# Performance work log

Measured on AMD Instinct MI355X. Metric: run time of the kernel, lower is better.

## Reference

```python
import jax, jax.numpy as jnp
import numpy as np

TOP_K = 2
HORIZON = 10


def _lstm_layer(seq, w_ih, w_hh, b_ih, b_hh):
    """Single torch-style LSTM layer over seq [T, in]; returns hidden seq [T, hid]."""
    hid = w_hh.shape[1]
    def step(carry, x_t):
        h, c = carry
        z = x_t @ w_ih.T + h @ w_hh.T + b_ih + b_hh  # [4*hid], torch gate order i,f,g,o
        i, f, g, o = jnp.split(z, 4)
        c = jax.nn.sigmoid(f) * c + jax.nn.sigmoid(i) * jnp.tanh(g)
        h = jax.nn.sigmoid(o) * jnp.tanh(c)
        return (h, c), h
    init = (jnp.zeros((hid,), seq.dtype), jnp.zeros((hid,), seq.dtype))
    _, hs = jax.lax.scan(step, init, seq)
    return hs


def setup_inputs() -> dict:
    key = jax.random.key(0)
    ks = jax.random.split(key, 12)
    H, E = 4096, 64
    B, S = 4, 4096
    s = 0.02
    return {
        "x": jax.random.normal(ks[0], (B, S, H), jnp.float32),
        "gate_w": jax.random.normal(ks[1], (E, H), jnp.float32) * s,
        "expert_bias": jnp.zeros((E,), jnp.float32),
        "cp_w1": jax.random.normal(ks[2], (64, H), jnp.float32) * s,
        "cp_b1": jnp.zeros((64,), jnp.float32),
        "cp_w2": jax.random.normal(ks[3], (1, 64), jnp.float32) * s,
        "cp_b2": jnp.zeros((1,), jnp.float32),
        "load_buffer": jax.random.uniform(ks[4], (50, E), jnp.float32),
        "lp_w_ih0": jax.random.normal(ks[5], (256, E), jnp.float32) * s,
        "lp_w_hh0": jax.random.normal(ks[6], (256, 64), jnp.float32) * s,
        "lp_b_ih0": jnp.zeros((256,), jnp.float32),
        "lp_b_hh0": jnp.zeros((256,), jnp.float32),
        "lp_w_ih1": jax.random.normal(ks[7], (256, 64), jnp.float32) * s,
        "lp_w_hh1": jax.random.normal(ks[8], (256, 64), jnp.float32) * s,
        "lp_b_ih1": jnp.zeros((256,), jnp.float32),
        "lp_b_hh1": jnp.zeros((256,), jnp.float32),
        "head_w": jax.random.normal(ks[9], (E * HORIZON, 64), jnp.float32) * s,
        "head_b": jnp.zeros((E * HORIZON,), jnp.float32),
    }


def reference(x, gate_w, expert_bias, cp_w1, cp_b1, cp_w2, cp_b2, load_buffer,
              lp_w_ih0, lp_w_hh0, lp_b_ih0, lp_b_hh0,
              lp_w_ih1, lp_w_hh1, lp_b_ih1, lp_b_hh1, head_w, head_b):
    sg = jax.lax.stop_gradient
    B, S, H = x.shape
    E = gate_w.shape[0]
    flat = x.reshape(-1, H)                       # [N, H]
    N = flat.shape[0]

    # --- routing logits (small gate GEMM) ---
    logits = flat @ gate_w.T                      # [N, E]

    # --- LSTM load prediction (torch.no_grad in original) ---
    seq = sg(load_buffer)
    h1 = _lstm_layer(seq, sg(lp_w_ih0), sg(lp_w_hh0), sg(lp_b_ih0), sg(lp_b_hh0))
    h2 = _lstm_layer(h1, sg(lp_w_ih1), sg(lp_w_hh1), sg(lp_b_ih1), sg(lp_b_hh1))
    pred = h2[-1] @ sg(head_w).T + sg(head_b)     # [E*HORIZON]
    future_load = jax.nn.softmax(pred.reshape(E, HORIZON).mean(axis=1))  # [E]

    # --- bias + predicted-load adjustment, softmax, top-k ---
    adj_logits = logits + expert_bias - sg(future_load)
    probs = jax.nn.softmax(adj_logits, axis=-1)   # [N, E]
    top_scores, top_idx = jax.lax.top_k(probs, TOP_K)
    top_scores = top_scores / top_scores.sum(axis=-1, keepdims=True)

    # --- switch-style load-balancing auxiliary loss ---
    one_hot = jax.nn.one_hot(top_idx, E, dtype=probs.dtype)   # [N, k, E]
    f = one_hot.sum(axis=(0, 1)) / (N * TOP_K)                # routed fraction per expert
    P = probs.mean(axis=0)                                    # mean routing prob
    aux_loss = E * jnp.sum(f * P)

    # --- dynamic capacity from complexity predictor (torch.no_grad) ---
    comp = jax.nn.sigmoid(
        jax.nn.relu(flat @ sg(cp_w1).T + sg(cp_b1)) @ sg(cp_w2).T + sg(cp_b2))  # [N,1]
    capacity = jnp.clip(0.5 + 1.5 * comp.mean(), 0.5, 2.0)

    return top_scores, top_idx, aux_loss, capacity, future_load
```

## Files before the change

### kernel.cpp

```cpp
#include <hip/hip_runtime.h>
#include <stdint.h>

#define IMG_OFF_BYTES 80000
#define CHUNK_IMG 16384
#define LOGITS_OFF 680000
#define TAU 1e-3f

#define XLOFF 5120
#define BUF_STRIDE 10240

typedef __attribute__((ext_vector_type(8))) short short8v;
typedef __attribute__((ext_vector_type(4))) short short4v;
typedef __attribute__((ext_vector_type(4))) float f32x4;

__device__ __forceinline__ float rlf(float v, int l) {
  return __int_as_float(__builtin_amdgcn_readlane(__float_as_int(v), l));
}
__device__ __forceinline__ float wsum(float v) {
#pragma unroll
  for (int o = 32; o; o >>= 1) v += __shfl_xor(v, o, 64);
  return v;
}
__device__ __forceinline__ float wmax(float v) {
#pragma unroll
  for (int o = 32; o; o >>= 1) v = fmaxf(v, __shfl_xor(v, o, 64));
  return v;
}
__device__ __forceinline__ unsigned short f2bf(float f) {
  unsigned u = __float_as_uint(f);
  u += 0x7fffu + ((u >> 16) & 1u);
  return (unsigned short)(u >> 16);
}
__device__ __forceinline__ float bf2f(unsigned short h) {
  return __uint_as_float(((unsigned)h) << 16);
}
__device__ __forceinline__ short8v frag8(const char* p0, const char* p1) {
  short4v a = *(const short4v*)p0;
  short4v b = *(const short4v*)p1;
  return __builtin_shufflevector(a, b, 0, 1, 2, 3, 4, 5, 6, 7);
}

__device__ __forceinline__ void lds_barrier() {
  asm volatile("s_waitcnt lgkmcnt(0)" ::: "memory");
  __builtin_amdgcn_s_barrier();
  asm volatile("" ::: "memory");
  __builtin_amdgcn_sched_barrier(0);
}

__global__ __launch_bounds__(256) void prep_kernel(
    const float* __restrict__ gate_w, const float* __restrict__ cp_w1,
    float* __restrict__ ws)
{
  const int c = blockIdx.x;
  const int tid = threadIdx.x;
  if (c == 0 && tid < 144) ws[64 + tid] = 0.f;
  {
    float4 z = make_float4(0.f, 0.f, 0.f, 0.f);
    float4* lz = (float4*)(ws + LOGITS_OFF + c * 16384);
#pragma unroll
    for (int i = 0; i < 16; ++i) lz[tid + i * 256] = z;
  }
  const int row = tid >> 1;
  const int half = tid & 1;
  const float* src = ((row < 64) ? (gate_w + (size_t)row * 4096)
                                 : (cp_w1 + (size_t)(row - 64) * 4096)) + c * 32 + half * 16;
  float v[16];
#pragma unroll
  for (int j = 0; j < 4; ++j) *(float4*)&v[j * 4] = *(const float4*)(src + j * 4);
  const int g = row >> 4, r15 = row & 15;
  char* img = (char*)ws + IMG_OFF_BYTES + (size_t)c * CHUNK_IMG + g * 2048;
#pragma unroll
  for (int q = 0; q < 4; ++q) {
    unsigned short h0 = f2bf(v[4 * q + 0]), h1 = f2bf(v[4 * q + 1]);
    unsigned short h2 = f2bf(v[4 * q + 2]), h3 = f2bf(v[4 * q + 3]);
    unsigned short l0 = f2bf(v[4 * q + 0] - bf2f(h0));
    unsigned short l1 = f2bf(v[4 * q + 1] - bf2f(h1));
    unsigned short l2 = f2bf(v[4 * q + 2] - bf2f(h2));
    unsigned short l3 = f2bf(v[4 * q + 3] - bf2f(h3));
    uint2 hv, lv;
    hv.x = (unsigned)h0 | ((unsigned)h1 << 16);
    hv.y = (unsigned)h2 | ((unsigned)h3 << 16);
    lv.x = (unsigned)l0 | ((unsigned)l1 << 16);
    lv.y = (unsigned)l2 | ((unsigned)l3 << 16);
    const int l = q * 16 + r15;
    *(uint2*)(img + l * 16 + half * 8) = hv;
    *(uint2*)(img + 1024 + l * 16 + half * 8) = lv;
  }
}

__device__ void lstm_device(
    char* ldsbase,
    const float* __restrict__ lb,
    const float* __restrict__ wih0, const float* __restrict__ whh0,
    const float* __restrict__ bih0, const float* __restrict__ bhh0,
    const float* __restrict__ wih1, const float* __restrict__ whh1,
    const float* __restrict__ bih1, const float* __restrict__ bhh1,
    const float* __restrict__ head_w, const float* __restrict__ head_b,
    float* __restrict__ ws, float* __restrict__ out, int N)
{
  float* seqh = (float*)ldsbase;
  float* h1s  = seqh + 3200;
  float* zbuf = h1s + 3200;
  float* hbuf = zbuf + 256;
  float* preds = hbuf + 64;
  const int tid = threadIdx.x;
  const int lane = tid & 63;
  for (int i = tid; i < 3200; i += 256) seqh[i] = lb[i];

  float hv = 0.f;
#pragma unroll 1
  for (int L = 0; L < 2; ++L) {
    const float* wip  = L ? wih1 : wih0;
    const float* whp  = L ? whh1 : whh0;
    const float* bip  = L ? bih1 : bih0;
    const float* bhp  = L ? bhh1 : bhh0;
    const float* seqp = L ? h1s  : seqh;
    float wiR[64], whR[64];
#pragma unroll
    for (int j = 0; j < 64; j += 4) {
      *(float4*)&wiR[j] = *(const float4*)(wip + tid * 64 + j);
      *(float4*)&whR[j] = *(const float4*)(whp + tid * 64 + j);
    }
    const float bsum = bip[tid] + bhp[tid];
    float c_reg = 0.f;
    hv = 0.f;
    if (tid < 64) hbuf[tid] = 0.f;
    __syncthreads();
#pragma unroll 1
    for (int t = 0; t < 50; ++t) {
      const float xv = seqp[t * 64 + lane];
      float a0 = bsum, a1 = 0.f, a2 = 0.f, a3 = 0.f;
#pragma unroll
      for (int j = 0; j < 64; j += 4) {
        a0 = fmaf(rlf(xv, j + 0), wiR[j + 0], a0);
        a1 = fmaf(rlf(xv, j + 1), wiR[j + 1], a1);
        a2 = fmaf(rlf(xv, j + 2), wiR[j + 2], a2);
        a3 = fmaf(rlf(xv, j + 3), wiR[j + 3], a3);
      }
#pragma unroll
      for (int j = 0; j < 64; j += 4) {
        a0 = fmaf(rlf(hv, j + 0), whR[j + 0], a0);
        a1 = fmaf(rlf(hv, j + 1), whR[j + 1], a1);
        a2 = fmaf(rlf(hv, j + 2), whR[j + 2], a2);
        a3 = fmaf(rlf(hv, j + 3), whR[j + 3], a3);
      }
      zbuf[tid] = (a0 + a1) + (a2 + a3);
      __syncthreads();
      if (tid < 64) {
        const float zi = zbuf[tid], zf = zbuf[64 + tid];
        const float zg = zbuf[128 + tid], zo = zbuf[192 + tid];
        const float si = 1.f / (1.f + expf(-zi));
        const float sf = 1.f / (1.f + expf(-zf));
        const float so = 1.f / (1.f + expf(-zo));
        c_reg = sf * c_reg + si * tanhf(zg);
        const float h = so * tanhf(c_reg);
        hbuf[tid] = h;
        if (L == 0) h1s[t * 64 + tid] = h;
      }
      __syncthreads();
      hv = hbuf[lane];
    }
    __syncthreads();
  }
  for (int o = tid; o < 640; o += 256) {
    const float* hw = head_w + o * 64;
    float a0 = 0.f, a1 = 0.f, a2 = 0.f, a3 = 0.f;
#pragma unroll
    for (int j = 0; j < 64; j += 4) {
      a0 = fmaf(rlf(hv, j + 0), hw[j + 0], a0);
      a1 = fmaf(rlf(hv, j + 1), hw[j + 1], a1);
      a2 = fmaf(rlf(hv, j + 2), hw[j + 2], a2);
      a3 = fmaf(rlf(hv, j + 3), hw[j + 3], a3);
    }
    preds[o] = (a0 + a1) + (a2 + a3) + head_b[o];
  }
  __syncthreads();
  if (tid < 64) {
    float m = 0.f;
#pragma unroll
    for (int h = 0; h < 10; ++h) m += preds[tid * 10 + h];
    m = m / 10.f;
    const float mx = wmax(m);
    const float p = expf(m - mx);
    const float s = wsum(p);
    const float flv = p / s;
    ws[tid] = flv;
    out[4 * N + 2 + tid] = flv;
  }
}

__global__ __launch_bounds__(256) void gemm_kernel(
    const float* __restrict__ x, float* __restrict__ ws, float* __restrict__ out,
    const float* __restrict__ lb,
    const float* __restrict__ wih0, const float* __restrict__ whh0,
    const float* __restrict__ bih0, const float* __restrict__ bhh0,
    const float* __restrict__ wih1, const float* __restrict__ whh1,
    const float* __restrict__ bih1, const float* __restrict__ bhh1,
    const float* __restrict__ head_w, const float* __restrict__ head_b,
    int N)
{
  __shared__ __align__(16) char lds[30720];
  if (blockIdx.x == 0) {
    lstm_device(lds, lb, wih0, whh0, bih0, bhh0, wih1, whh1, bih1, bhh1,
                head_w, head_b, ws, out, N);
    return;
  }
  const int b = blockIdx.x - 1;
  const int tb = (b & 255) * 64;
  const int ck0 = (b >> 8) * 32;
  const int tid = threadIdx.x;
  const int lane = tid & 63;
  const int wv = __builtin_amdgcn_readfirstlane(tid >> 6);
  const int r15 = lane & 15;
  const int fo = (lane >> 4) * 8;
  const int row = tid >> 2;
  const int kslot = tid & 3;
  const float* xsrc = x + (size_t)(tb + row) * 4096 + kslot * 8;
  const char* wimg = (const char*)ws + IMG_OFF_BYTES;
  char* buf0 = lds;
  char* buf1 = lds + BUF_STRIDE;

  f32x4 acc[4][2];
#pragma unroll
  for (int mi = 0; mi < 4; ++mi)
#pragma unroll
    for (int ni = 0; ni < 2; ++ni) acc[mi][ni] = (f32x4)0.f;

  float xa[8], xb[8];
  short8v whA[2], wlA[2], whB[2], wlB[2];

#define LOADX(R, C)                                                        \
  { *(float4*)&R[0] = *(const float4*)(xsrc + (size_t)(C) * 32);           \
    *(float4*)&R[4] = *(const float4*)(xsrc + (size_t)(C) * 32 + 4); }

#define WRITEX(R, BASE)                                                    \
  { uint4 hv, lv; unsigned hu[4], lu[4];                                   \
    _Pragma("unroll")                                                      \
    for (int i = 0; i < 4; ++i) {                                          \
      unsigned short h0 = f2bf(R[2 * i]), h1 = f2bf(R[2 * i + 1]);         \
      unsigned short l0 = f2bf(R[2 * i] - bf2f(h0));                       \
      unsigned short l1 = f2bf(R[2 * i + 1] - bf2f(h1));                   \
      hu[i] = (unsigned)h0 | ((unsigned)h1 << 16);                         \
      lu[i] = (unsigned)l0 | ((unsigned)l1 << 16);                         \
    }                                                                      \
    hv.x = hu[0]; hv.y = hu[1]; hv.z = hu[2]; hv.w = hu[3];                \
    lv.x = lu[0]; lv.y = lu[1]; lv.z = lu[2]; lv.w = lu[3];                \
    *(uint4*)((BASE) + row * 80 + kslot * 16) = hv;                        \
    *(uint4*)((BASE) + XLOFF + row * 80 + kslot * 16) = lv; }

#define WLOADR(C, WH, WL)                                                  \
  { const char* wb = wimg + (size_t)(C) * CHUNK_IMG + wv * 4096 + lane * 16; \
    WH[0] = *(const short8v*)wb;                                           \
    WL[0] = *(const short8v*)(wb + 1024);                                  \
    WH[1] = *(const short8v*)(wb + 2048);                                  \
    WL[1] = *(const short8v*)(wb + 3072); }

#define COMPUTE(BASE, WH, WL)                                              \
  { short8v xh[4], xl[4];                                                  \
    _Pragma("unroll")                                                      \
    for (int mi = 0; mi < 4; ++mi) {                                       \
      const char* p = (BASE) + (mi * 16 + r15) * 80 + fo;                  \
      xh[mi] = frag8(p, p + 32);                                           \
      xl[mi] = frag8(p + XLOFF, p + XLOFF + 32);                           \
    }                                                                      \
    _Pragma("unroll")                                                      \
    for (int mi = 0; mi < 4; ++mi)                                         \
      _Pragma("unroll")                                                    \
      for (int ni = 0; ni < 2; ++ni) {                                     \
        acc[mi][ni] = __builtin_amdgcn_mfma_f32_16x16x32_bf16(             \
            xh[mi], WH[ni], acc[mi][ni], 0, 0, 0);                         \
        acc[mi][ni] = __builtin_amdgcn_mfma_f32_16x16x32_bf16(             \
            xh[mi], WL[ni], acc[mi][ni], 0, 0, 0);                         \
        acc[mi][ni] = __builtin_amdgcn_mfma_f32_16x16x32_bf16(             \
            xl[mi], WH[ni], acc[mi][ni], 0, 0, 0);                         \
      } }

  LOADX(xa, ck0);
  LOADX(xb, ck0 + 1);
  WLOADR(ck0, whA, wlA);
  WRITEX(xa, buf0);
  lds_barrier();

#pragma unroll 1
  for (int cc = 0; cc < 16; ++cc) {
    const int c0 = ck0 + 2 * cc, c1 = c0 + 1;
    WLOADR(c1, whB, wlB);
    if (cc < 15) LOADX(xa, c0 + 2);
    COMPUTE(buf0, whA, wlA);
    WRITEX(xb, buf1);
    lds_barrier();
    if (cc < 15) WLOADR(c0 + 2, whA, wlA);
    if (cc < 15) LOADX(xb, c1 + 2);
    COMPUTE(buf1, whB, wlB);
    if (cc < 15) WRITEX(xa, buf0);
    lds_barrier();
  }

  float* lg = ws + LOGITS_OFF;
#pragma unroll
  for (int mi = 0; mi < 4; ++mi)
#pragma unroll
    for (int ni = 0; ni < 2; ++ni)
#pragma unroll
      for (int r = 0; r < 4; ++r) {
        const int tokrow = tb + mi * 16 + (lane >> 4) * 4 + r;
        const int col = wv * 32 + ni * 16 + r15;
        atomicAdd(&lg[(size_t)tokrow * 128 + col], acc[mi][ni][r]);
      }
#undef LOADX
#undef WRITEX
#undef WLOADR
#undef COMPUTE
}

__global__ __launch_bounds__(256) void epi_kernel(
    const float* __restrict__ eb_p, const float* __restrict__ cp_b1,
    const float* __restrict__ cp_w2, const float* __restrict__ cp_b2,
    float* __restrict__ ws, float* __restrict__ out, int N)
{
  const int tid = threadIdx.x;
  const int lane = tid & 63;
  const int wv = __builtin_amdgcn_readfirstlane(tid >> 6);
  const int tb = blockIdx.x * 32;
  const float* lg = ws + LOGITS_OFF;
  int* qd = (int*)(ws + 200);
  __shared__ float sP[64];
  __shared__ float scnt[64];
  __shared__ float scomp;
  if (tid < 64) { sP[tid] = 0.f; scnt[tid] = 0.f; }
  if (tid == 0) scomp = 0.f;
  __syncthreads();

  const float eb = eb_p[lane];
  const float fl = ws[lane];
  const float cb1 = cp_b1[lane];
  const float cw2 = cp_w2[lane];
  const float cb2 = cp_b2[0];
  float psum_local = 0.f, comp_local = 0.f;
  float* o_ts = out;
  float* o_ti = out + 2 * N;

#pragma unroll 1
  for (int tt = 0; tt < 8; ++tt) {
    const int tok = tb + wv * 8 + tt;
    const float lgv = lg[(size_t)tok * 128 + lane];
    const float lc  = lg[(size_t)tok * 128 + 64 + lane];
    float rr = fmaxf(lc + cb1, 0.f) * cw2;
    rr = wsum(rr);
    const float comp = 1.f / (1.f + expf(-(rr + cb2)));
    comp_local += comp;
    const float a = lgv + eb - fl;
    float m1 = a; int i1 = lane;
#pragma unroll
    for (int o = 32; o; o >>= 1) {
      const float ov = __shfl_xor(m1, o, 64);
      const int oi = __shfl_xor(i1, o, 64);
      if (ov > m1 || (ov == m1 && oi < i1)) { m1 = ov; i1 = oi; }
    }
    float m2 = (lane == i1) ? -1e30f : a; int i2 = lane;
#pragma unroll
    for (int o = 32; o; o >>= 1) {
      const float ov = __shfl_xor(m2, o, 64);
      const int oi = __shfl_xor(i2, o, 64);
      if (ov > m2 || (ov == m2 && oi < i2)) { m2 = ov; i2 = oi; }
    }
    float m3 = (lane == i1 || lane == i2) ? -1e30f : a;
#pragma unroll
    for (int o = 32; o; o >>= 1) m3 = fmaxf(m3, __shfl_xor(m3, o, 64));
    const float p = expf(a - m1);
    const float ssum = wsum(p);
    const float prob = p / ssum;
    psum_local += prob;
    const float s1 = rlf(prob, i1);
    const float s2 = rlf(prob, i2);
    if (lane == 0) {
      const float inv = 1.f / (s1 + s2);
      o_ts[tok * 2 + 0] = s1 * inv;
      o_ts[tok * 2 + 1] = s2 * inv;
      o_ti[tok * 2 + 0] = (float)i1;
      o_ti[tok * 2 + 1] = (float)i2;
      atomicAdd(&scnt[i1], 1.f);
      atomicAdd(&scnt[i2], 1.f);
      if (m1 - m2 < TAU || m2 - m3 < TAU) {
        int slot = atomicAdd(qd, 1);
        qd[8 + slot] = tok;
      }
    }
  }
  atomicAdd(&sP[lane], psum_local);
  if (lane == 0) atomicAdd(&scomp, comp_local);
  __syncthreads();
  if (tid < 64) {
    atomicAdd(&ws[64 + tid], sP[tid]);
    atomicAdd(&ws[128 + tid], scnt[tid]);
  }
  if (tid == 0) atomicAdd(&ws[192], scomp);
}

__global__ __launch_bounds__(256) void repair_kernel(
    const float* __restrict__ x, const float* __restrict__ gate_w,
    const float* __restrict__ eb_p, float* __restrict__ ws,
    float* __restrict__ out, int N)
{
  const int tid = threadIdx.x;
  __shared__ float red[256];
  int* qd = (int*)(ws + 200);
  const int qn = qd[0];
  float* o_ts = out;
  float* o_ti = out + 2 * N;

  for (int e = blockIdx.x; e < qn; e += gridDim.x) {
    const int tok = qd[8 + e];
    const int o = tid & 63;
    const int kq = tid >> 6;
    const float* xr = x + (size_t)tok * 4096 + kq * 1024;
    const float* wr = gate_w + (size_t)o * 4096 + kq * 1024;
    float s = 0.f;
#pragma unroll 4
    for (int j = 0; j < 256; ++j) {
      const float4 xv = *(const float4*)(xr + j * 4);
      const float4 wv = *(const float4*)(wr + j * 4);
      s = fmaf(xv.x, wv.x, s); s = fmaf(xv.y, wv.y, s);
      s = fmaf(xv.z, wv.z, s); s = fmaf(xv.w, wv.w, s);
    }
    red[tid] = s;
    __syncthreads();
    if (tid < 64) {
      const float a = red[tid] + red[64 + tid] + red[128 + tid] +
                      red[192 + tid] + eb_p[tid] - ws[tid];
      const int lane = tid;
      float m1 = a; int i1 = lane;
#pragma unroll
      for (int oo = 32; oo; oo >>= 1) {
        const float ov = __shfl_xor(m1, oo, 64);
        const int oi = __shfl_xor(i1, oo, 64);
        if (ov > m1 || (ov == m1 && oi < i1)) { m1 = ov; i1 = oi; }
      }
      float m2 = (lane == i1) ? -1e30f : a; int i2 = lane;
#pragma unroll
      for (int oo = 32; oo; oo >>= 1) {
        const float ov = __shfl_xor(m2, oo, 64);
        const int oi = __shfl_xor(i2, oo, 64);
        if (ov > m2 || (ov == m2 && oi < i2)) { m2 = ov; i2 = oi; }
      }
      const float p = expf(a - m1);
      const float ssum = wsum(p);
      const float s1 = rlf(p, i1) / ssum;
      const float s2 = rlf(p, i2) / ssum;
      if (lane == 0) {
        const int i1o = (int)o_ti[tok * 2 + 0];
        const int i2o = (int)o_ti[tok * 2 + 1];
        const float inv = 1.f / (s1 + s2);
        o_ts[tok * 2 + 0] = s1 * inv;
        o_ts[tok * 2 + 1] = s2 * inv;
        o_ti[tok * 2 + 0] = (float)i1;
        o_ti[tok * 2 + 1] = (float)i2;
        if (i1o != i1 || i2o != i2) {
          atomicAdd(&ws[128 + i1o], -1.f);
          atomicAdd(&ws[128 + i2o], -1.f);
          atomicAdd(&ws[128 + i1], 1.f);
          atomicAdd(&ws[128 + i2], 1.f);
        }
      }
    }
    __syncthreads();
  }
}

__global__ __launch_bounds__(64) void fin_kernel(const float* __restrict__ ws,
                                                 float* __restrict__ out, int N) {
  const int e = threadIdx.x;
  const float P = ws[64 + e] / (float)N;
  const float f = ws[128 + e] / (float)(2 * N);
  const float v = wsum(f * P);
  if (e == 0) {
    out[4 * N + 0] = 64.f * v;
    float cap = 0.5f + 1.5f * (ws[192] / (float)N);
    out[4 * N + 1] = fminf(fmaxf(cap, 0.5f), 2.f);
  }
}

extern "C" void kernel_launch(void* const* d_in, const int* in_sizes, int n_in,
                              void* d_out, int out_size, void* d_ws, size_t ws_size,
                              hipStream_t stream) {
  const float* x          = (const float*)d_in[0];
  const float* gate_w     = (const float*)d_in[1];
  const float* expert_bias= (const float*)d_in[2];
  const float* cp_w1      = (const float*)d_in[3];
  const float* cp_b1      = (const float*)d_in[4];
  const float* cp_w2      = (const float*)d_in[5];
  const float* cp_b2      = (const float*)d_in[6];
  const float* load_buffer= (const float*)d_in[7];
  const float* wih0       = (const float*)d_in[8];
  const float* whh0       = (const float*)d_in[9];
  const float* bih0       = (const float*)d_in[10];
  const float* bhh0       = (const float*)d_in[11];
  const float* wih1       = (const float*)d_in[12];
  const float* whh1       = (const float*)d_in[13];
  const float* bih1       = (const float*)d_in[14];
  const float* bhh1       = (const float*)d_in[15];
  const float* head_w     = (const float*)d_in[16];
  const float* head_b     = (const float*)d_in[17];
  float* out = (float*)d_out;
  float* ws  = (float*)d_ws;
  const int N = in_sizes[0] / 4096;

  prep_kernel<<<128, 256, 0, stream>>>(gate_w, cp_w1, ws);
  gemm_kernel<<<1025, 256, 0, stream>>>(x, ws, out, load_buffer,
                                        wih0, whh0, bih0, bhh0,
                                        wih1, whh1, bih1, bhh1,
                                        head_w, head_b, N);
  epi_kernel<<<N / 32, 256, 0, stream>>>(expert_bias, cp_b1, cp_w2, cp_b2,
                                         ws, out, N);
  repair_kernel<<<128, 256, 0, stream>>>(x, gate_w, expert_bias, ws, out, N);
  fin_kernel<<<1, 64, 0, stream>>>(ws, out, N);
}
```

Baseline: 203.0 us.

## Replace split-K atomic accumulation with per-split slabs reduced in epilogue

Each GEMM block now stages its partial 64x128 tile in LDS and writes it with coalesced float4 stores into a per-K-split slab, instead of issuing scalar global atomicAdds. The epilogue sums the four slabs when it reads the logits. This also removes the zeroing pass in the prep kernel. The cost is four times the workspace for logits, four reads per value in the epilogue, and extra LDS use per block.

```diff
diff --git a/kernel.cpp b/kernel.cpp
--- a/kernel.cpp
+++ b/kernel.cpp
@@ -4,6 +4,7 @@
 #define IMG_OFF_BYTES 80000
 #define CHUNK_IMG 16384
 #define LOGITS_OFF 680000
+#define SLAB 2097152
 #define TAU 1e-3f
 
 #define XLOFF 5120
@@ -54,12 +55,6 @@
   const int c = blockIdx.x;
   const int tid = threadIdx.x;
   if (c == 0 && tid < 144) ws[64 + tid] = 0.f;
-  {
-    float4 z = make_float4(0.f, 0.f, 0.f, 0.f);
-    float4* lz = (float4*)(ws + LOGITS_OFF + c * 16384);
-#pragma unroll
-    for (int i = 0; i < 16; ++i) lz[tid + i * 256] = z;
-  }
   const int row = tid >> 1;
   const int half = tid & 1;
   const float* src = ((row < 64) ? (gate_w + (size_t)row * 4096)
@@ -199,7 +194,7 @@
     const float* __restrict__ head_w, const float* __restrict__ head_b,
     int N)
 {
-  __shared__ __align__(16) char lds[30720];
+  __shared__ __align__(16) char lds[34048];
   if (blockIdx.x == 0) {
     lstm_device(lds, lb, wih0, whh0, bih0, bhh0, wih1, whh1, bih1, bhh1,
                 head_w, head_b, ws, out, N);
@@ -207,7 +202,8 @@
   }
   const int b = blockIdx.x - 1;
   const int tb = (b & 255) * 64;
-  const int ck0 = (b >> 8) * 32;
+  const int kq = b >> 8;
+  const int ck0 = kq * 32;
   const int tid = threadIdx.x;
   const int lane = tid & 63;
   const int wv = __builtin_amdgcn_readfirstlane(tid >> 6);
@@ -296,17 +292,24 @@
     lds_barrier();
   }
 
-  float* lg = ws + LOGITS_OFF;
+  float (*souts)[132] = (float(*)[132])lds;
 #pragma unroll
   for (int mi = 0; mi < 4; ++mi)
 #pragma unroll
     for (int ni = 0; ni < 2; ++ni)
 #pragma unroll
-      for (int r = 0; r < 4; ++r) {
-        const int tokrow = tb + mi * 16 + (lane >> 4) * 4 + r;
-        const int col = wv * 32 + ni * 16 + r15;
-        atomicAdd(&lg[(size_t)tokrow * 128 + col], acc[mi][ni][r]);
-      }
+      for (int r = 0; r < 4; ++r)
+        souts[mi * 16 + (lane >> 4) * 4 + r][wv * 32 + ni * 16 + r15] =
+            acc[mi][ni][r];
+  lds_barrier();
+  {
+    float* slab = ws + LOGITS_OFF + (size_t)kq * SLAB;
+    const int srow = tid >> 2, sq = tid & 3;
+    float4* dst = (float4*)(slab + (size_t)(tb + srow) * 128 + sq * 32);
+    const float4* srcp = (const float4*)&souts[srow][sq * 32];
+#pragma unroll
+    for (int i = 0; i < 8; ++i) dst[i] = srcp[i];
+  }
 #undef LOADX
 #undef WRITEX
 #undef WLOADR
@@ -343,8 +346,11 @@
 #pragma unroll 1
   for (int tt = 0; tt < 8; ++tt) {
     const int tok = tb + wv * 8 + tt;
-    const float lgv = lg[(size_t)tok * 128 + lane];
-    const float lc  = lg[(size_t)tok * 128 + 64 + lane];
+    const size_t base = (size_t)tok * 128;
+    const float lgv = ((lg[base + lane] + lg[SLAB + base + lane]) +
+                       (lg[2 * SLAB + base + lane] + lg[3 * SLAB + base + lane]));
+    const float lc  = ((lg[base + 64 + lane] + lg[SLAB + base + 64 + lane]) +
+                       (lg[2 * SLAB + base + 64 + lane] + lg[3 * SLAB + base + 64 + lane]));
     float rr = fmaxf(lc + cb1, 0.f) * cw2;
     rr = wsum(rr);
     const float comp = 1.f / (1.f + expf(-(rr + cb2)));
```

After: 216.6 us. 1.07x slower.
